# Kernel tuning notes

Hardware: AMD Instinct MI355X
Metric: run time of the kernel (lower is better)

The kernel has to match this reference:

```python
import jax, jax.numpy as jnp
import numpy as np
from jax import lax

N_REF = 500000   # reference cohort size
N_PC = 128       # PCA components
N_FEAT = 2000    # raw feature dim
TOP_K = 16


def setup_inputs() -> dict:
    key = jax.random.key(0)
    k1, k2, k3, k4 = jax.random.split(key, 4)
    data_in = jax.random.normal(k1, (1, N_FEAT), dtype=jnp.float32)
    transform_mat = jax.random.normal(k2, (N_FEAT, N_PC), dtype=jnp.float32)
    ref_data = jax.random.normal(k3, (N_REF, N_PC), dtype=jnp.float32)
    psuedo = jax.random.uniform(k4, (N_REF,), dtype=jnp.float32)
    return {
        "data_in": data_in,
        "transform_mat": transform_mat,
        "ref_data": ref_data,
        "psuedo": psuedo,
        "K": TOP_K,
    }


def reference(data_in, transform_mat, ref_data, psuedo, K):
    # project query into PCA space: [1, P]
    data_in_pc = jnp.matmul(data_in, transform_mat)
    # L1 distance to every reference sample: [N]
    dist = jnp.sum(jnp.abs(data_in_pc - ref_data), axis=1)
    # K nearest neighbors (smallest distances); ties irrelevant for mean
    _, top_k_ind = lax.top_k(-dist, K)
    inference_score = jnp.mean(psuedo[top_k_ind])
    return inference_score[None]  # shape [1], matches tf.expand_dims
```

## Files before the change

kernel.cpp:

```cpp
#include <hip/hip_runtime.h>
#include <stdint.h>

#define N_REF   500000
#define N_PC    128
#define N_FEAT  2000
#define TOPK    16

#define K1_BLOCKS  2048
#define K1_THREADS 256
#define K1_WAVES   (K1_BLOCKS * (K1_THREADS / 64))
#define N_QUAD     (N_REF / 4)

#define PROJ_BLOCKS 40
#define FEAT_PER_BLK 50

#define K2_BLOCKS  128
#define NCAND      (K2_BLOCKS * TOPK)

typedef unsigned long long u64;

__device__ __forceinline__ void insert16(u64* top, u64 x) {
#pragma unroll
    for (int i = 15; i >= 1; --i) {
        u64 lo = top[i - 1];
        u64 hi = (x > lo) ? x : lo;
        top[i] = (top[i] < hi) ? top[i] : hi;
    }
    top[0] = (top[0] < x) ? top[0] : x;
}

__device__ __forceinline__ u64 bitonic_sort64(u64 v, int lane) {
#pragma unroll
    for (int k = 2; k <= 64; k <<= 1) {
#pragma unroll
        for (int j = k >> 1; j >= 1; j >>= 1) {
            u64 o = __shfl_xor(v, j);
            bool up    = ((lane & k) == 0);
            bool lower = ((lane & j) == 0);
            u64 mn = (v < o) ? v : o;
            u64 mx = (v < o) ? o : v;
            v = (up == lower) ? mn : mx;
        }
    }
    return v;
}

__global__ void proj_partial(const float* __restrict__ din,
                             const float* __restrict__ T,
                             float* __restrict__ part) {
    int b = blockIdx.x;
    int t = threadIdx.x;
    int f0 = b * FEAT_PER_BLK;
    float acc = 0.f;
#pragma unroll 10
    for (int i = 0; i < FEAT_PER_BLK; ++i) {
        int f = f0 + i;
        acc += din[f] * T[(size_t)f * N_PC + t];
    }
    part[b * N_PC + t] = acc;
}

__global__ __launch_bounds__(K1_THREADS) void dist_stream(
        const float* __restrict__ part,
        const float* __restrict__ ref,
        float* __restrict__ dist) {
    __shared__ __align__(16) float pc[N_PC];

    int tid  = threadIdx.x;
    int lane = tid & 63;
    int w    = tid >> 6;

    if (tid < N_PC) {
        float s = 0.f;
#pragma unroll
        for (int b = 0; b < PROJ_BLOCKS; ++b) s += part[b * N_PC + tid];
        pc[tid] = s;
    }
    __syncthreads();

    float4 qv = reinterpret_cast<const float4*>(pc)[lane & 31];

    int gw = blockIdx.x * (K1_THREADS / 64) + w;
    const float4* ref4 = reinterpret_cast<const float4*>(ref);

    for (int g = gw; g < N_QUAD; g += K1_WAVES) {
        size_t base = (size_t)g * 128;
        float4 va = ref4[base + lane];
        float4 vb = ref4[base + 64 + lane];
        float d0 = fabsf(qv.x - va.x) + fabsf(qv.y - va.y)
                 + fabsf(qv.z - va.z) + fabsf(qv.w - va.w);
        float d1 = fabsf(qv.x - vb.x) + fabsf(qv.y - vb.y)
                 + fabsf(qv.z - vb.z) + fabsf(qv.w - vb.w);
#pragma unroll
        for (int off = 16; off >= 1; off >>= 1) {
            d0 += __shfl_xor(d0, off);
            d1 += __shfl_xor(d1, off);
        }
        if ((lane & 31) == 0) {
            int half = lane >> 5;
            dist[4 * g + half]     = d0;
            dist[4 * g + 2 + half] = d1;
        }
    }
}

__global__ __launch_bounds__(256) void topk_dist(
        const float* __restrict__ dist,
        u64* __restrict__ cand) {
    __shared__ u64 wl[64];
    int tid  = threadIdx.x;
    int lane = tid & 63;
    int w    = tid >> 6;

    u64 top[TOPK];
#pragma unroll
    for (int i = 0; i < TOPK; ++i) top[i] = ~0ull;

    for (int i = blockIdx.x * 256 + tid; i < N_REF; i += K2_BLOCKS * 256) {
        u64 key = (((u64)(unsigned)__float_as_int(dist[i])) << 32) | (unsigned)i;
        if (key < top[TOPK - 1]) insert16(top, key);
    }

    u64 chosen = 0;
#pragma unroll
    for (int r = 0; r < TOPK; ++r) {
        u64 m = top[0];
#pragma unroll
        for (int off = 32; off >= 1; off >>= 1) {
            u64 o = __shfl_xor(m, off);
            m = (o < m) ? o : m;
        }
        if (top[0] == m) {
#pragma unroll
            for (int i = 0; i < TOPK - 1; ++i) top[i] = top[i + 1];
            top[TOPK - 1] = ~0ull;
        }
        if (lane == r) chosen = m;
    }
    if (lane < TOPK) wl[w * TOPK + lane] = chosen;
    __syncthreads();

    if (tid < 64) {
        u64 v = bitonic_sort64(wl[tid], tid);
        if (tid < TOPK) cand[blockIdx.x * TOPK + tid] = v;
    }
}

__global__ __launch_bounds__(256) void final_topk(
        const u64* __restrict__ cand,
        const float* __restrict__ psuedo,
        float* __restrict__ out) {
    __shared__ u64 wl[64];
    int tid  = threadIdx.x;
    int lane = tid & 63;
    int w    = tid >> 6;

    u64 top[TOPK];
#pragma unroll
    for (int i = 0; i < TOPK; ++i) top[i] = ~0ull;

    for (int i = tid; i < NCAND; i += 256) {
        u64 x = cand[i];
        if (x < top[TOPK - 1]) insert16(top, x);
    }

    u64 chosen = 0;
#pragma unroll
    for (int r = 0; r < TOPK; ++r) {
        u64 m = top[0];
#pragma unroll
        for (int off = 32; off >= 1; off >>= 1) {
            u64 o = __shfl_xor(m, off);
            m = (o < m) ? o : m;
        }
        if (top[0] == m) {
#pragma unroll
            for (int i = 0; i < TOPK - 1; ++i) top[i] = top[i + 1];
            top[TOPK - 1] = ~0ull;
        }
        if (lane == r) chosen = m;
    }
    if (lane < TOPK) wl[w * TOPK + lane] = chosen;
    __syncthreads();

    if (tid < 64) {
        u64 v = bitonic_sort64(wl[tid], tid);
        float p = 0.f;
        if (tid < TOPK) p = psuedo[(unsigned)(v & 0xffffffffull)];
#pragma unroll
        for (int off = 32; off >= 1; off >>= 1)
            p += __shfl_xor(p, off);
        if (tid == 0) out[0] = p * (1.0f / (float)TOPK);
    }
}

extern "C" void kernel_launch(void* const* d_in, const int* in_sizes, int n_in,
                              void* d_out, int out_size, void* d_ws, size_t ws_size,
                              hipStream_t stream) {
    const float* din = (const float*)d_in[0];
    const float* T   = (const float*)d_in[1];
    const float* ref = (const float*)d_in[2];
    const float* ps  = (const float*)d_in[3];

    float* part = (float*)d_ws;
    float* dist = (float*)((char*)d_ws + 32768);
    u64*   cand = (u64*)((char*)d_ws + 32768 + N_REF * 4);
    float* outp = (float*)d_out;

    proj_partial<<<PROJ_BLOCKS, 128, 0, stream>>>(din, T, part);
    dist_stream<<<K1_BLOCKS, K1_THREADS, 0, stream>>>(part, ref, dist);
    topk_dist<<<K2_BLOCKS, 256, 0, stream>>>(dist, cand);
    final_topk<<<1, 256, 0, stream>>>(cand, ps, outp);
}
```

Baseline: 394.1 us.

## Fuse final top-k into block top-k via atomic ticket, unroll distance loop

Merges the final top-k reduction into the per-block top-k kernel. The last block to finish, detected with an atomic counter that the projection kernel resets, does the final merge, which removes one kernel launch. It also processes two row-groups per iteration in the distance kernel for more loads in flight, vectorizes distance reads in the top-k pass with float4, and changes the projection split to 16 blocks of 125 features. The risks are a serial tail in the last block and higher register pressure from the occupancy hint.

New measurement: 406.7 us. 3.2% more time.

```diff
diff --git a/kernel.cpp b/kernel.cpp
--- a/kernel.cpp
+++ b/kernel.cpp
@@ -11,8 +11,8 @@
 #define K1_WAVES   (K1_BLOCKS * (K1_THREADS / 64))
 #define N_QUAD     (N_REF / 4)
 
-#define PROJ_BLOCKS 40
-#define FEAT_PER_BLK 50
+#define PROJ_BLOCKS 16
+#define FEAT_PER_BLK 125
 
 #define K2_BLOCKS  128
 #define NCAND      (K2_BLOCKS * TOPK)
@@ -45,14 +45,36 @@
     return v;
 }
 
+__device__ __forceinline__ u64 wave_minpop16(u64* top, int lane) {
+    u64 chosen = 0;
+#pragma unroll
+    for (int r = 0; r < TOPK; ++r) {
+        u64 m = top[0];
+#pragma unroll
+        for (int off = 32; off >= 1; off >>= 1) {
+            u64 o = __shfl_xor(m, off);
+            m = (o < m) ? o : m;
+        }
+        if (top[0] == m) {
+#pragma unroll
+            for (int i = 0; i < TOPK - 1; ++i) top[i] = top[i + 1];
+            top[TOPK - 1] = ~0ull;
+        }
+        if (lane == r) chosen = m;
+    }
+    return chosen;
+}
+
 __global__ void proj_partial(const float* __restrict__ din,
                              const float* __restrict__ T,
-                             float* __restrict__ part) {
+                             float* __restrict__ part,
+                             unsigned* __restrict__ counter) {
+    if (blockIdx.x == 0 && threadIdx.x == 0) *counter = 0u;
     int b = blockIdx.x;
     int t = threadIdx.x;
     int f0 = b * FEAT_PER_BLK;
     float acc = 0.f;
-#pragma unroll 10
+#pragma unroll 5
     for (int i = 0; i < FEAT_PER_BLK; ++i) {
         int f = f0 + i;
         acc += din[f] * T[(size_t)f * N_PC + t];
@@ -60,7 +82,7 @@
     part[b * N_PC + t] = acc;
 }
 
-__global__ __launch_bounds__(K1_THREADS) void dist_stream(
+__global__ __launch_bounds__(K1_THREADS, 8) void dist_stream(
         const float* __restrict__ part,
         const float* __restrict__ ref,
         float* __restrict__ dist) {
@@ -83,7 +105,39 @@
     int gw = blockIdx.x * (K1_THREADS / 64) + w;
     const float4* ref4 = reinterpret_cast<const float4*>(ref);
 
-    for (int g = gw; g < N_QUAD; g += K1_WAVES) {
+    int g = gw;
+    for (; g + K1_WAVES < N_QUAD; g += 2 * K1_WAVES) {
+        int g2 = g + K1_WAVES;
+        size_t b0 = (size_t)g  * 128;
+        size_t b1 = (size_t)g2 * 128;
+        float4 va = ref4[b0 + lane];
+        float4 vb = ref4[b0 + 64 + lane];
+        float4 vc = ref4[b1 + lane];
+        float4 vd = ref4[b1 + 64 + lane];
+        float d0 = fabsf(qv.x - va.x) + fabsf(qv.y - va.y)
+                 + fabsf(qv.z - va.z) + fabsf(qv.w - va.w);
+        float d1 = fabsf(qv.x - vb.x) + fabsf(qv.y - vb.y)
+                 + fabsf(qv.z - vb.z) + fabsf(qv.w - vb.w);
+        float d2 = fabsf(qv.x - vc.x) + fabsf(qv.y - vc.y)
+                 + fabsf(qv.z - vc.z) + fabsf(qv.w - vc.w);
+        float d3 = fabsf(qv.x - vd.x) + fabsf(qv.y - vd.y)
+                 + fabsf(qv.z - vd.z) + fabsf(qv.w - vd.w);
+#pragma unroll
+        for (int off = 16; off >= 1; off >>= 1) {
+            d0 += __shfl_xor(d0, off);
+            d1 += __shfl_xor(d1, off);
+            d2 += __shfl_xor(d2, off);
+            d3 += __shfl_xor(d3, off);
+        }
+        if ((lane & 31) == 0) {
+            int half = lane >> 5;
+            dist[4 * g  + half]     = d0;
+            dist[4 * g  + 2 + half] = d1;
+            dist[4 * g2 + half]     = d2;
+            dist[4 * g2 + 2 + half] = d3;
+        }
+    }
+    for (; g < N_QUAD; g += K1_WAVES) {
         size_t base = (size_t)g * 128;
         float4 va = ref4[base + lane];
         float4 vb = ref4[base + 64 + lane];
@@ -104,10 +158,14 @@
     }
 }
 
-__global__ __launch_bounds__(256) void topk_dist(
+__global__ __launch_bounds__(256) void topk_fused(
         const float* __restrict__ dist,
-        u64* __restrict__ cand) {
+        const float* __restrict__ psuedo,
+        u64* __restrict__ cand,
+        unsigned* __restrict__ counter,
+        float* __restrict__ out) {
     __shared__ u64 wl[64];
+    __shared__ unsigned s_ticket;
     int tid  = threadIdx.x;
     int lane = tid & 63;
     int w    = tid >> 6;
@@ -116,27 +174,21 @@
 #pragma unroll
     for (int i = 0; i < TOPK; ++i) top[i] = ~0ull;
 
-    for (int i = blockIdx.x * 256 + tid; i < N_REF; i += K2_BLOCKS * 256) {
-        u64 key = (((u64)(unsigned)__float_as_int(dist[i])) << 32) | (unsigned)i;
-        if (key < top[TOPK - 1]) insert16(top, key);
-    }
-
-    u64 chosen = 0;
-#pragma unroll
-    for (int r = 0; r < TOPK; ++r) {
-        u64 m = top[0];
-#pragma unroll
-        for (int off = 32; off >= 1; off >>= 1) {
-            u64 o = __shfl_xor(m, off);
-            m = (o < m) ? o : m;
-        }
-        if (top[0] == m) {
-#pragma unroll
-            for (int i = 0; i < TOPK - 1; ++i) top[i] = top[i + 1];
-            top[TOPK - 1] = ~0ull;
-        }
-        if (lane == r) chosen = m;
-    }
+    const float4* dist4 = reinterpret_cast<const float4*>(dist);
+    for (int i = blockIdx.x * 256 + tid; i < N_REF / 4; i += K2_BLOCKS * 256) {
+        float4 v = dist4[i];
+        unsigned base = 4u * (unsigned)i;
+        u64 k0 = (((u64)(unsigned)__float_as_int(v.x)) << 32) | (base + 0u);
+        u64 k1 = (((u64)(unsigned)__float_as_int(v.y)) << 32) | (base + 1u);
+        u64 k2 = (((u64)(unsigned)__float_as_int(v.z)) << 32) | (base + 2u);
+        u64 k3 = (((u64)(unsigned)__float_as_int(v.w)) << 32) | (base + 3u);
+        if (k0 < top[TOPK - 1]) insert16(top, k0);
+        if (k1 < top[TOPK - 1]) insert16(top, k1);
+        if (k2 < top[TOPK - 1]) insert16(top, k2);
+        if (k3 < top[TOPK - 1]) insert16(top, k3);
+    }
+
+    u64 chosen = wave_minpop16(top, lane);
     if (lane < TOPK) wl[w * TOPK + lane] = chosen;
     __syncthreads();
 
@@ -144,42 +196,23 @@
         u64 v = bitonic_sort64(wl[tid], tid);
         if (tid < TOPK) cand[blockIdx.x * TOPK + tid] = v;
     }
-}
-
-__global__ __launch_bounds__(256) void final_topk(
-        const u64* __restrict__ cand,
-        const float* __restrict__ psuedo,
-        float* __restrict__ out) {
-    __shared__ u64 wl[64];
-    int tid  = threadIdx.x;
-    int lane = tid & 63;
-    int w    = tid >> 6;
-
-    u64 top[TOPK];
+
+    __threadfence();
+    __syncthreads();
+    if (tid == 0) s_ticket = atomicAdd(counter, 1u);
+    __syncthreads();
+    if (s_ticket != K2_BLOCKS - 1) return;
+
+    __threadfence();
 #pragma unroll
     for (int i = 0; i < TOPK; ++i) top[i] = ~0ull;
-
-    for (int i = tid; i < NCAND; i += 256) {
-        u64 x = cand[i];
+#pragma unroll
+    for (int r = 0; r < NCAND / 256; ++r) {
+        u64 x = cand[r * 256 + tid];
         if (x < top[TOPK - 1]) insert16(top, x);
     }
-
-    u64 chosen = 0;
-#pragma unroll
-    for (int r = 0; r < TOPK; ++r) {
-        u64 m = top[0];
-#pragma unroll
-        for (int off = 32; off >= 1; off >>= 1) {
-            u64 o = __shfl_xor(m, off);
-            m = (o < m) ? o : m;
-        }
-        if (top[0] == m) {
-#pragma unroll
-            for (int i = 0; i < TOPK - 1; ++i) top[i] = top[i + 1];
-            top[TOPK - 1] = ~0ull;
-        }
-        if (lane == r) chosen = m;
-    }
+    chosen = wave_minpop16(top, lane);
+    __syncthreads();
     if (lane < TOPK) wl[w * TOPK + lane] = chosen;
     __syncthreads();
 
@@ -202,13 +235,14 @@
     const float* ref = (const float*)d_in[2];
     const float* ps  = (const float*)d_in[3];
 
-    float* part = (float*)d_ws;
-    float* dist = (float*)((char*)d_ws + 32768);
-    u64*   cand = (u64*)((char*)d_ws + 32768 + N_REF * 4);
-    float* outp = (float*)d_out;
-
-    proj_partial<<<PROJ_BLOCKS, 128, 0, stream>>>(din, T, part);
+    char* ws = (char*)d_ws;
+    float*    part    = (float*)ws;
+    float*    dist    = (float*)(ws + 32768);
+    u64*      cand    = (u64*)(ws + 32768 + N_REF * 4);
+    unsigned* counter = (unsigned*)(ws + 32768 + N_REF * 4 + NCAND * 8);
+    float*    outp    = (float*)d_out;
+
+    proj_partial<<<PROJ_BLOCKS, 128, 0, stream>>>(din, T, part, counter);
     dist_stream<<<K1_BLOCKS, K1_THREADS, 0, stream>>>(part, ref, dist);
-    topk_dist<<<K2_BLOCKS, 256, 0, stream>>>(dist, cand);
-    final_topk<<<1, 256, 0, stream>>>(cand, ps, outp);
-}
+    topk_fused<<<K2_BLOCKS, 256, 0, stream>>>(dist, ps, cand, counter, outp);
+}
```
